# Optimization experiments

Measured on AMD Instinct MI355X. Metric: run time of the kernel, lower is better.

The kernel has to match this reference:

```python
import jax, jax.numpy as jnp
import numpy as np

N = 1_000_000   # nodes
E = 32_000_000  # directed edges (avg degree 32)


def setup_inputs() -> dict:
    key = jax.random.key(0)
    k1, k2, k3 = jax.random.split(key, 3)
    x = jax.random.normal(k1, (N, 1), dtype=jnp.float32)
    edge_index = jax.random.randint(k2, (2, E), 0, N, dtype=jnp.int32)
    W = jax.random.normal(k3, (1, 1), dtype=jnp.float32) * 0.5
    b = jnp.zeros((1,), dtype=jnp.float32)
    return {"x": x, "edge_index": edge_index, "W": W, "b": b}


def reference(x, edge_index, W, b):
    # GCNConv with default add_self_loops=True, normalize=True, then sigmoid.
    n = x.shape[0]
    loops = jnp.arange(n, dtype=edge_index.dtype)
    src = jnp.concatenate([edge_index[0], loops])  # [E+N]
    dst = jnp.concatenate([edge_index[1], loops])  # [E+N]

    # degree over destination nodes (self-loops included -> deg >= 1)
    deg = jax.ops.segment_sum(jnp.ones_like(dst, dtype=x.dtype), dst, num_segments=n)
    dinv = jax.lax.rsqrt(deg)                      # [N]
    norm = dinv[src] * dinv[dst]                   # [E+N] symmetric normalization

    xw = x @ W                                     # [N, 1] linear transform
    msg = xw[src] * norm[:, None]                  # gather + scale, [E+N, 1]
    agg = jax.ops.segment_sum(msg, dst, num_segments=n)  # scatter-add, [N, 1]
    return jax.nn.sigmoid(agg + b)
```

## Files before the change

kernel.cpp:

```cpp
#include <hip/hip_runtime.h>
#include <math.h>

typedef unsigned int u32;
typedef unsigned long long u64;
typedef int iv4 __attribute__((ext_vector_type(4)));
typedef float fv4 __attribute__((ext_vector_type(4)));

#define BKT_BITS 12
#define BKT_SIZE 4096
#define NBMAX    256
#define DEPTH    31
#define BIN_T    256
#define TILE     4096
#define SPLIT    4
#define HA_T     512
#define OVFCAP   131072u


__global__ void zero_u32(u32* __restrict__ p, int n) {
    int i = blockIdx.x * blockDim.x + threadIdx.x;
    if (i < n) p[i] = 0u;
}

__global__ void __launch_bounds__(BIN_T)
bin_kernel5(const int* __restrict__ src, const int* __restrict__ dst,
            u32* __restrict__ recs, u32* __restrict__ gcursor,
            u32* __restrict__ ovfcnt, u32* __restrict__ ovf,
            int E, int NB, u32 CAP) {
    __shared__ u32 stag[NBMAX * DEPTH];
    __shared__ u32 scnt[NBMAX];
    int tid = threadIdx.x;
    for (int t = tid; t < NBMAX; t += BIN_T) scnt[t] = 0u;
    __syncthreads();
    int base = blockIdx.x * TILE;
#pragma unroll
    for (int r = 0; r < TILE / (BIN_T * 4); ++r) {
        int v  = (base >> 2) + r * BIN_T + tid;
        int e0 = v << 2;
        if (e0 + 3 < E) {
            iv4 s4 = __builtin_nontemporal_load(reinterpret_cast<const iv4*>(src) + v);
            iv4 d4 = __builtin_nontemporal_load(reinterpret_cast<const iv4*>(dst) + v);
#pragma unroll
            for (int k = 0; k < 4; ++k) {
                u32 ss = (u32)s4[k], dd = (u32)d4[k];
                u32 b   = dd >> BKT_BITS;
                u32 rec = (ss << BKT_BITS) | (dd & (BKT_SIZE - 1));
                u32 slot = atomicAdd(&scnt[b], 1u);
                if (slot < DEPTH) stag[b * DEPTH + slot] = rec;
                else {
                    u32 g = atomicAdd(&gcursor[b], 1u);
                    if (g < CAP) recs[(size_t)b * CAP + g] = rec;
                    else {
                        u32 oi = atomicAdd(ovfcnt, 1u);
                        if (oi < OVFCAP) { ovf[2u*oi] = ss; ovf[2u*oi+1u] = dd; }
                    }
                }
            }
        } else if (e0 < E) {
            for (int e = e0; e < E && e < e0 + 4; ++e) {
                u32 ss = (u32)src[e], dd = (u32)dst[e];
                u32 b   = dd >> BKT_BITS;
                u32 rec = (ss << BKT_BITS) | (dd & (BKT_SIZE - 1));
                u32 slot = atomicAdd(&scnt[b], 1u);
                if (slot < DEPTH) stag[b * DEPTH + slot] = rec;
                else {
                    u32 g = atomicAdd(&gcursor[b], 1u);
                    if (g < CAP) recs[(size_t)b * CAP + g] = rec;
                    else {
                        u32 oi = atomicAdd(ovfcnt, 1u);
                        if (oi < OVFCAP) { ovf[2u*oi] = ss; ovf[2u*oi+1u] = dd; }
                    }
                }
            }
        }
    }
    __syncthreads();
    int t = tid;
    if (t < NB) {
        u32 c = scnt[t]; if (c > DEPTH) c = DEPTH;
        if (c > 0u) {
            u32 g = atomicAdd(&gcursor[t], c);
            size_t bp = (size_t)t * CAP;
            if (g + c <= CAP) {
                for (u32 k = 0; k < c; ++k) recs[bp + g + k] = stag[t * DEPTH + k];
            } else {
                for (u32 k = 0; k < c; ++k) {
                    u32 rec = stag[t * DEPTH + k];
                    u32 pos = g + k;
                    if (pos < CAP) recs[bp + pos] = rec;
                    else {
                        u32 oi = atomicAdd(ovfcnt, 1u);
                        if (oi < OVFCAP) {
                            ovf[2u*oi]    = rec >> BKT_BITS;
                            ovf[2u*oi+1u] = ((u32)t << BKT_BITS) | (rec & (BKT_SIZE - 1));
                        }
                    }
                }
            }
        }
    }
}

__global__ void __launch_bounds__(HA_T, 8)
hist_kernel(const u32* __restrict__ recs, const u32* __restrict__ gcursor,
            const u32* __restrict__ ovfcnt, const u32* __restrict__ ovf,
            u32* __restrict__ deg, u32 CAP) {
    __shared__ u32 hh[BKT_SIZE];
    int tid = threadIdx.x;
    int b = blockIdx.x >> 2;
    int split = blockIdx.x & 3;
    for (int j = tid; j < BKT_SIZE; j += HA_T) hh[j] = 0u;
    if (blockIdx.x == 0) {
        u32 on = *ovfcnt; if (on > OVFCAP) on = OVFCAP;
        for (u32 k = tid; k < on; k += HA_T) atomicAdd(&deg[ovf[2u*k+1u]], 1u);
    }
    __syncthreads();
    u32 cnt = gcursor[b]; if (cnt > CAP) cnt = CAP;
    u32 chunk = (((cnt + SPLIT - 1) / SPLIT) + 3u) & ~3u;
    u32 start = split * chunk; if (start > cnt) start = cnt;
    u32 end = start + chunk;   if (end > cnt)   end = cnt;
    const u32* rp = recs + (size_t)b * CAP;
    u32 nv = (end - start) >> 2;
    const iv4* rp4 = reinterpret_cast<const iv4*>(rp + start);
    for (u32 v = tid; v < nv; v += HA_T) {
        iv4 r = __builtin_nontemporal_load(rp4 + v);
        atomicAdd(&hh[((u32)r.x) & (BKT_SIZE - 1)], 1u);
        atomicAdd(&hh[((u32)r.y) & (BKT_SIZE - 1)], 1u);
        atomicAdd(&hh[((u32)r.z) & (BKT_SIZE - 1)], 1u);
        atomicAdd(&hh[((u32)r.w) & (BKT_SIZE - 1)], 1u);
    }
    for (u32 k = start + (nv << 2) + tid; k < end; k += HA_T)
        atomicAdd(&hh[rp[k] & (BKT_SIZE - 1)], 1u);
    __syncthreads();
    int nid0 = b << BKT_BITS;
    for (int j = tid; j < BKT_SIZE; j += HA_T) {
        u32 v = hh[j];
        if (v) atomicAdd(&deg[nid0 + j], v);
    }
}

__global__ void node_kernel2(const float* __restrict__ x, u32* __restrict__ degacc,
                             const float* __restrict__ W,
                             float* __restrict__ dinv, float* __restrict__ s, int N) {
    int i = (blockIdx.x * blockDim.x + threadIdx.x) << 2;
    float W0 = W[0];
    if (i + 3 < N) {
        iv4 d  = *reinterpret_cast<const iv4*>(degacc + i);
        fv4 xv = *reinterpret_cast<const fv4*>(x + i);
        fv4 dv, sv;
#pragma unroll
        for (int j = 0; j < 4; ++j) {
            float di = rsqrtf((float)((u32)d[j] + 1u));
            dv[j] = di;
            sv[j] = xv[j] * W0 * di;
        }
        *reinterpret_cast<fv4*>(dinv + i) = dv;
        *reinterpret_cast<fv4*>(s + i)    = sv;
        *reinterpret_cast<fv4*>(reinterpret_cast<float*>(degacc) + i) = sv;
    } else {
        for (; i < N; ++i) {
            u32 d = degacc[i];
            float di = rsqrtf((float)(d + 1u));
            float si = x[i] * W0 * di;
            dinv[i] = di; s[i] = si;
            reinterpret_cast<float*>(degacc)[i] = si;
        }
    }
}

__global__ void __launch_bounds__(HA_T, 8)
agg_kernel(const u32* __restrict__ recs, const u32* __restrict__ gcursor,
           const u32* __restrict__ ovfcnt, const u32* __restrict__ ovf,
           const float* __restrict__ s, float* __restrict__ acc, u32 CAP) {
    __shared__ float aa[BKT_SIZE];
    int tid = threadIdx.x;
    int b = blockIdx.x >> 2;
    int split = blockIdx.x & 3;
    for (int j = tid; j < BKT_SIZE; j += HA_T) aa[j] = 0.0f;
    if (blockIdx.x == 0) {
        u32 on = *ovfcnt; if (on > OVFCAP) on = OVFCAP;
        for (u32 k = tid; k < on; k += HA_T)
            atomicAdd(&acc[ovf[2u*k+1u]], s[ovf[2u*k]]);
    }
    __syncthreads();
    u32 cnt = gcursor[b]; if (cnt > CAP) cnt = CAP;
    u32 chunk = (((cnt + SPLIT - 1) / SPLIT) + 3u) & ~3u;
    u32 start = split * chunk; if (start > cnt) start = cnt;
    u32 end = start + chunk;   if (end > cnt)   end = cnt;
    const u32* rp = recs + (size_t)b * CAP;
    u32 nv = (end - start) >> 2;
    const iv4* rp4 = reinterpret_cast<const iv4*>(rp + start);
    for (u32 v = tid; v < nv; v += HA_T) {
        iv4 r = __builtin_nontemporal_load(rp4 + v);
        atomicAdd(&aa[((u32)r.x) & (BKT_SIZE - 1)], s[((u32)r.x) >> BKT_BITS]);
        atomicAdd(&aa[((u32)r.y) & (BKT_SIZE - 1)], s[((u32)r.y) >> BKT_BITS]);
        atomicAdd(&aa[((u32)r.z) & (BKT_SIZE - 1)], s[((u32)r.z) >> BKT_BITS]);
        atomicAdd(&aa[((u32)r.w) & (BKT_SIZE - 1)], s[((u32)r.w) >> BKT_BITS]);
    }
    for (u32 k = start + (nv << 2) + tid; k < end; k += HA_T) {
        u32 r = rp[k];
        atomicAdd(&aa[r & (BKT_SIZE - 1)], s[r >> BKT_BITS]);
    }
    __syncthreads();
    int nid0 = b << BKT_BITS;
    for (int j = tid; j < BKT_SIZE; j += HA_T) {
        float v = aa[j];
        if (v != 0.0f) atomicAdd(&acc[nid0 + j], v);
    }
}

__global__ void out_kernel2(const u32* __restrict__ degacc, const float* __restrict__ dinv,
                            const float* __restrict__ bb, float* __restrict__ out, int N) {
    int i = (blockIdx.x * blockDim.x + threadIdx.x) << 2;
    float b0 = bb[0];
    const float* accf = reinterpret_cast<const float*>(degacc);
    if (i + 3 < N) {
        fv4 a  = *reinterpret_cast<const fv4*>(accf + i);
        fv4 dv = *reinterpret_cast<const fv4*>(dinv + i);
        fv4 o;
#pragma unroll
        for (int j = 0; j < 4; ++j) {
            float z = dv[j] * a[j] + b0;
            o[j] = 1.0f / (1.0f + expf(-z));
        }
        *reinterpret_cast<fv4*>(out + i) = o;
    } else {
        for (; i < N; ++i) {
            float z = dinv[i] * accf[i] + b0;
            out[i] = 1.0f / (1.0f + expf(-z));
        }
    }
}

__global__ void zero_kernel(int* __restrict__ p, int n) {
    int i = blockIdx.x * blockDim.x + threadIdx.x;
    if (i < n) p[i] = 0;
}
__global__ void deg_kernel(const int* __restrict__ dst, int* __restrict__ deg, int E) {
    int i = (blockIdx.x * blockDim.x + threadIdx.x) * 4;
    if (i + 3 < E) {
        int4 d = *reinterpret_cast<const int4*>(dst + i);
        atomicAdd(&deg[d.x], 1); atomicAdd(&deg[d.y], 1);
        atomicAdd(&deg[d.z], 1); atomicAdd(&deg[d.w], 1);
    } else {
        for (int k = i; k < E; ++k) atomicAdd(&deg[dst[k]], 1);
    }
}
__global__ void node_kernel(const float* __restrict__ x, const int* __restrict__ deg,
                            const float* __restrict__ W, float* __restrict__ s,
                            float* __restrict__ dinv, float* __restrict__ acc, int N) {
    int i = blockIdx.x * blockDim.x + threadIdx.x;
    if (i < N) {
        float di = rsqrtf((float)(deg[i] + 1));
        float si = x[i] * W[0] * di;
        dinv[i] = di; s[i] = si; acc[i] = si;
    }
}
__global__ void scatter_kernel(const int* __restrict__ src, const int* __restrict__ dst,
                               const float* __restrict__ s, float* __restrict__ acc, int E) {
    int i = (blockIdx.x * blockDim.x + threadIdx.x) * 4;
    if (i + 3 < E) {
        int4 sv = *reinterpret_cast<const int4*>(src + i);
        int4 dv = *reinterpret_cast<const int4*>(dst + i);
        atomicAdd(&acc[dv.x], s[sv.x]); atomicAdd(&acc[dv.y], s[sv.y]);
        atomicAdd(&acc[dv.z], s[sv.z]); atomicAdd(&acc[dv.w], s[sv.w]);
    } else {
        for (int k = i; k < E; ++k) atomicAdd(&acc[dst[k]], s[src[k]]);
    }
}
__global__ void out_kernel(const float* __restrict__ acc, const float* __restrict__ dinv,
                           const float* __restrict__ b, float* __restrict__ out, int N) {
    int i = blockIdx.x * blockDim.x + threadIdx.x;
    if (i < N) {
        float z = dinv[i] * acc[i] + b[0];
        out[i] = 1.0f / (1.0f + expf(-z));
    }
}

extern "C" void kernel_launch(void* const* d_in, const int* in_sizes, int n_in,
                              void* d_out, int out_size, void* d_ws, size_t ws_size,
                              hipStream_t stream) {
    const int N = in_sizes[0];
    const int E = in_sizes[1] / 2;
    const float* x  = (const float*)d_in[0];
    const int*   ei = (const int*)d_in[1];
    const float* W  = (const float*)d_in[2];
    const float* b  = (const float*)d_in[3];
    float* out = (float*)d_out;

    const int* srcp = ei;
    const int* dstp = ei + E;
    const int T = 256;

    const int NB = (N + BKT_SIZE - 1) >> BKT_BITS;
    u64 meanCnt = (N > 0) ? (((u64)E << BKT_BITS) / (u64)N) : 0ull;
    const u32 CAP = (u32)((meanCnt + 2048ull + 63ull) & ~63ull);
    const size_t recCap   = (size_t)NB * CAP;
    const size_t off_cur  = recCap;
    const size_t off_ovfc = off_cur + NBMAX;
    const size_t off_ovf  = off_ovfc + 16;
    const size_t off_deg  = off_ovf + 2 * (size_t)OVFCAP;
    const size_t off_dinv = off_deg + (size_t)N;
    const size_t off_s    = off_dinv + (size_t)N;
    const size_t need = (off_s + (size_t)N) * 4;

    if (N <= (1 << 20) && NB <= NBMAX && (N & 15) == 0 && (E & 3) == 0 &&
        E > 0 && ws_size >= need) {
        u32* p = (u32*)d_ws;
        u32*   recs    = p;
        u32*   gcursor = p + off_cur;
        u32*   ovfcnt  = p + off_ovfc;
        u32*   ovf     = p + off_ovf;
        u32*   deg     = p + off_deg;
        float* dinv    = (float*)(p + off_dinv);
        float* s       = (float*)(p + off_s);

        zero_u32<<<(NBMAX + 16 + T - 1) / T, T, 0, stream>>>(gcursor, NBMAX + 16);
        zero_u32<<<(N + T - 1) / T, T, 0, stream>>>(deg, N);
        bin_kernel5<<<(E + TILE - 1) / TILE, BIN_T, 0, stream>>>(
            srcp, dstp, recs, gcursor, ovfcnt, ovf, E, NB, CAP);
        hist_kernel<<<NB * SPLIT, HA_T, 0, stream>>>(recs, gcursor, ovfcnt, ovf, deg, CAP);
        node_kernel2<<<((N + 3) / 4 + T - 1) / T, T, 0, stream>>>(x, deg, W, dinv, s, N);
        agg_kernel<<<NB * SPLIT, HA_T, 0, stream>>>(
            recs, gcursor, ovfcnt, ovf, s, (float*)deg, CAP);
        out_kernel2<<<((N + 3) / 4 + T - 1) / T, T, 0, stream>>>(deg, dinv, b, out, N);
    } else {
        char* ws = (char*)d_ws;
        int*   deg  = (int*)ws;
        float* s    = (float*)(ws + (size_t)N * 4);
        float* dinv = (float*)(ws + (size_t)N * 8);
        float* acc  = (float*)deg;
        const int blocksN = (N + T - 1) / T;
        const int blocksE = ((E + 3) / 4 + T - 1) / T;
        zero_kernel<<<blocksN, T, 0, stream>>>(deg, N);
        deg_kernel<<<blocksE, T, 0, stream>>>(dstp, deg, E);
        node_kernel<<<blocksN, T, 0, stream>>>(x, deg, W, s, dinv, acc, N);
        scatter_kernel<<<blocksE, T, 0, stream>>>(srcp, dstp, s, acc, E);
        out_kernel<<<blocksN, T, 0, stream>>>(acc, dinv, b, out, N);
    }
}
```

Before: 670.3 us.

## Fold degree counting into binning kernel and unroll aggregation gathers

Removes the separate histogram kernel by having the binning kernel atomically increment global degree per edge, saving a full re-read of the binned records. The aggregation loop is unrolled four-way so that sixteen gathers of s are issued before their LDS atomics, to raise memory-level parallelism. The trade is 32M scattered global atomics in the bin pass instead of LDS-local counting.

```diff
diff --git a/kernel.cpp b/kernel.cpp
--- a/kernel.cpp
+++ b/kernel.cpp
@@ -23,9 +23,10 @@
 }
 
 __global__ void __launch_bounds__(BIN_T)
-bin_kernel5(const int* __restrict__ src, const int* __restrict__ dst,
+bin_kernel6(const int* __restrict__ src, const int* __restrict__ dst,
             u32* __restrict__ recs, u32* __restrict__ gcursor,
             u32* __restrict__ ovfcnt, u32* __restrict__ ovf,
+            u32* __restrict__ deg,
             int E, int NB, u32 CAP) {
     __shared__ u32 stag[NBMAX * DEPTH];
     __shared__ u32 scnt[NBMAX];
@@ -43,6 +44,7 @@
 #pragma unroll
             for (int k = 0; k < 4; ++k) {
                 u32 ss = (u32)s4[k], dd = (u32)d4[k];
+                atomicAdd(&deg[dd], 1u);
                 u32 b   = dd >> BKT_BITS;
                 u32 rec = (ss << BKT_BITS) | (dd & (BKT_SIZE - 1));
                 u32 slot = atomicAdd(&scnt[b], 1u);
@@ -59,6 +61,7 @@
         } else if (e0 < E) {
             for (int e = e0; e < E && e < e0 + 4; ++e) {
                 u32 ss = (u32)src[e], dd = (u32)dst[e];
+                atomicAdd(&deg[dd], 1u);
                 u32 b   = dd >> BKT_BITS;
                 u32 rec = (ss << BKT_BITS) | (dd & (BKT_SIZE - 1));
                 u32 slot = atomicAdd(&scnt[b], 1u);
@@ -101,44 +104,6 @@
     }
 }
 
-__global__ void __launch_bounds__(HA_T, 8)
-hist_kernel(const u32* __restrict__ recs, const u32* __restrict__ gcursor,
-            const u32* __restrict__ ovfcnt, const u32* __restrict__ ovf,
-            u32* __restrict__ deg, u32 CAP) {
-    __shared__ u32 hh[BKT_SIZE];
-    int tid = threadIdx.x;
-    int b = blockIdx.x >> 2;
-    int split = blockIdx.x & 3;
-    for (int j = tid; j < BKT_SIZE; j += HA_T) hh[j] = 0u;
-    if (blockIdx.x == 0) {
-        u32 on = *ovfcnt; if (on > OVFCAP) on = OVFCAP;
-        for (u32 k = tid; k < on; k += HA_T) atomicAdd(&deg[ovf[2u*k+1u]], 1u);
-    }
-    __syncthreads();
-    u32 cnt = gcursor[b]; if (cnt > CAP) cnt = CAP;
-    u32 chunk = (((cnt + SPLIT - 1) / SPLIT) + 3u) & ~3u;
-    u32 start = split * chunk; if (start > cnt) start = cnt;
-    u32 end = start + chunk;   if (end > cnt)   end = cnt;
-    const u32* rp = recs + (size_t)b * CAP;
-    u32 nv = (end - start) >> 2;
-    const iv4* rp4 = reinterpret_cast<const iv4*>(rp + start);
-    for (u32 v = tid; v < nv; v += HA_T) {
-        iv4 r = __builtin_nontemporal_load(rp4 + v);
-        atomicAdd(&hh[((u32)r.x) & (BKT_SIZE - 1)], 1u);
-        atomicAdd(&hh[((u32)r.y) & (BKT_SIZE - 1)], 1u);
-        atomicAdd(&hh[((u32)r.z) & (BKT_SIZE - 1)], 1u);
-        atomicAdd(&hh[((u32)r.w) & (BKT_SIZE - 1)], 1u);
-    }
-    for (u32 k = start + (nv << 2) + tid; k < end; k += HA_T)
-        atomicAdd(&hh[rp[k] & (BKT_SIZE - 1)], 1u);
-    __syncthreads();
-    int nid0 = b << BKT_BITS;
-    for (int j = tid; j < BKT_SIZE; j += HA_T) {
-        u32 v = hh[j];
-        if (v) atomicAdd(&deg[nid0 + j], v);
-    }
-}
-
 __global__ void node_kernel2(const float* __restrict__ x, u32* __restrict__ degacc,
                              const float* __restrict__ W,
                              float* __restrict__ dinv, float* __restrict__ s, int N) {
@@ -190,7 +155,38 @@
     const u32* rp = recs + (size_t)b * CAP;
     u32 nv = (end - start) >> 2;
     const iv4* rp4 = reinterpret_cast<const iv4*>(rp + start);
-    for (u32 v = tid; v < nv; v += HA_T) {
+    u32 v = tid;
+    for (; v + 3u * HA_T < nv; v += 4u * HA_T) {
+        iv4 r0 = __builtin_nontemporal_load(rp4 + v);
+        iv4 r1 = __builtin_nontemporal_load(rp4 + v + HA_T);
+        iv4 r2 = __builtin_nontemporal_load(rp4 + v + 2u * HA_T);
+        iv4 r3 = __builtin_nontemporal_load(rp4 + v + 3u * HA_T);
+        float g0  = s[((u32)r0.x) >> BKT_BITS], g1  = s[((u32)r0.y) >> BKT_BITS];
+        float g2  = s[((u32)r0.z) >> BKT_BITS], g3  = s[((u32)r0.w) >> BKT_BITS];
+        float g4  = s[((u32)r1.x) >> BKT_BITS], g5  = s[((u32)r1.y) >> BKT_BITS];
+        float g6  = s[((u32)r1.z) >> BKT_BITS], g7  = s[((u32)r1.w) >> BKT_BITS];
+        float g8  = s[((u32)r2.x) >> BKT_BITS], g9  = s[((u32)r2.y) >> BKT_BITS];
+        float g10 = s[((u32)r2.z) >> BKT_BITS], g11 = s[((u32)r2.w) >> BKT_BITS];
+        float g12 = s[((u32)r3.x) >> BKT_BITS], g13 = s[((u32)r3.y) >> BKT_BITS];
+        float g14 = s[((u32)r3.z) >> BKT_BITS], g15 = s[((u32)r3.w) >> BKT_BITS];
+        atomicAdd(&aa[((u32)r0.x) & (BKT_SIZE - 1)], g0);
+        atomicAdd(&aa[((u32)r0.y) & (BKT_SIZE - 1)], g1);
+        atomicAdd(&aa[((u32)r0.z) & (BKT_SIZE - 1)], g2);
+        atomicAdd(&aa[((u32)r0.w) & (BKT_SIZE - 1)], g3);
+        atomicAdd(&aa[((u32)r1.x) & (BKT_SIZE - 1)], g4);
+        atomicAdd(&aa[((u32)r1.y) & (BKT_SIZE - 1)], g5);
+        atomicAdd(&aa[((u32)r1.z) & (BKT_SIZE - 1)], g6);
+        atomicAdd(&aa[((u32)r1.w) & (BKT_SIZE - 1)], g7);
+        atomicAdd(&aa[((u32)r2.x) & (BKT_SIZE - 1)], g8);
+        atomicAdd(&aa[((u32)r2.y) & (BKT_SIZE - 1)], g9);
+        atomicAdd(&aa[((u32)r2.z) & (BKT_SIZE - 1)], g10);
+        atomicAdd(&aa[((u32)r2.w) & (BKT_SIZE - 1)], g11);
+        atomicAdd(&aa[((u32)r3.x) & (BKT_SIZE - 1)], g12);
+        atomicAdd(&aa[((u32)r3.y) & (BKT_SIZE - 1)], g13);
+        atomicAdd(&aa[((u32)r3.z) & (BKT_SIZE - 1)], g14);
+        atomicAdd(&aa[((u32)r3.w) & (BKT_SIZE - 1)], g15);
+    }
+    for (; v < nv; v += HA_T) {
         iv4 r = __builtin_nontemporal_load(rp4 + v);
         atomicAdd(&aa[((u32)r.x) & (BKT_SIZE - 1)], s[((u32)r.x) >> BKT_BITS]);
         atomicAdd(&aa[((u32)r.y) & (BKT_SIZE - 1)], s[((u32)r.y) >> BKT_BITS]);
@@ -204,8 +200,8 @@
     __syncthreads();
     int nid0 = b << BKT_BITS;
     for (int j = tid; j < BKT_SIZE; j += HA_T) {
-        float v = aa[j];
-        if (v != 0.0f) atomicAdd(&acc[nid0 + j], v);
+        float vv = aa[j];
+        if (vv != 0.0f) atomicAdd(&acc[nid0 + j], vv);
     }
 }
 
@@ -317,9 +313,8 @@
 
         zero_u32<<<(NBMAX + 16 + T - 1) / T, T, 0, stream>>>(gcursor, NBMAX + 16);
         zero_u32<<<(N + T - 1) / T, T, 0, stream>>>(deg, N);
-        bin_kernel5<<<(E + TILE - 1) / TILE, BIN_T, 0, stream>>>(
-            srcp, dstp, recs, gcursor, ovfcnt, ovf, E, NB, CAP);
-        hist_kernel<<<NB * SPLIT, HA_T, 0, stream>>>(recs, gcursor, ovfcnt, ovf, deg, CAP);
+        bin_kernel6<<<(E + TILE - 1) / TILE, BIN_T, 0, stream>>>(
+            srcp, dstp, recs, gcursor, ovfcnt, ovf, deg, E, NB, CAP);
         node_kernel2<<<((N + 3) / 4 + T - 1) / T, T, 0, stream>>>(x, deg, W, dinv, s, N);
         agg_kernel<<<NB * SPLIT, HA_T, 0, stream>>>(
             recs, gcursor, ovfcnt, ovf, s, (float*)deg, CAP);
```

After: 1.811 ms. 2.7x slower.
